# Optimization experiments

Hardware: AMD Instinct MI355X
Metric: run time of the kernel (lower is better)

## Reference

```python
import jax, jax.numpy as jnp
import numpy as np

D = 1024
H = 16
HD = D // H
SCALE = HD ** -0.5
EPS = 1e-5


def _layernorm(x, g, b):
    mu = jnp.mean(x, axis=-1, keepdims=True)
    var = jnp.var(x, axis=-1, keepdims=True)
    return (x - mu) * jax.lax.rsqrt(var + EPS) * g + b


def setup_inputs() -> dict:
    key = jax.random.key(0)
    ks = jax.random.split(key, 10)
    B, L = 2, 2048
    x = jax.random.normal(ks[0], (B, L, D), dtype=jnp.float32)
    s = 1.0 / np.sqrt(D)
    w_qkv = jax.random.normal(ks[1], (D, 3 * D), dtype=jnp.float32) * s
    w_out = jax.random.normal(ks[2], (D, D), dtype=jnp.float32) * s
    w1 = jax.random.normal(ks[3], (D, 2 * D), dtype=jnp.float32) * s
    b1 = jnp.zeros((2 * D,), dtype=jnp.float32)
    w2 = jax.random.normal(ks[4], (2 * D, D), dtype=jnp.float32) / np.sqrt(2 * D)
    b2 = jnp.zeros((D,), dtype=jnp.float32)
    g1 = jnp.ones((D,), dtype=jnp.float32)
    be1 = jnp.zeros((D,), dtype=jnp.float32)
    g2 = jnp.ones((D,), dtype=jnp.float32)
    be2 = jnp.zeros((D,), dtype=jnp.float32)
    return {"x": x, "w_qkv": w_qkv, "w_out": w_out, "w1": w1, "b1": b1,
            "w2": w2, "b2": b2, "g1": g1, "be1": be1, "g2": g2, "be2": be2}


def reference(x, w_qkv, w_out, w1, b1, w2, b2, g1, be1, g2, be2):
    B, L, _ = x.shape
    qkv = (x @ w_qkv).reshape(B, L, 3, H, HD)
    q, k, v = jnp.moveaxis(qkv, 2, 0)          # each [B, L, H, HD]
    # scores: [B, H, L, L]
    attn = jnp.einsum('bqhd,bkhd->bhqk', q, k) * SCALE
    causal = jnp.tril(jnp.ones((L, L), dtype=bool))
    attn = jnp.where(causal[None, None], attn, -jnp.inf)
    attn = jax.nn.softmax(attn, axis=-1)
    out = jnp.einsum('bhqk,bkhd->bqhd', attn, v).reshape(B, L, D)
    out = out @ w_out
    x = _layernorm(x + out, g1, be1)
    ffn = jax.nn.gelu(x @ w1 + b1, approximate=False) @ w2 + b2
    x = _layernorm(x + ffn, g2, be2)
    return x
```

## Files before the change

### kernel.cpp

```cpp
#include <hip/hip_runtime.h>
#include <hip/hip_bf16.h>
#include <math.h>

#define L_SEQ 2048
#define NB 2
#define DM 1024
#define NHEAD 16
#define HDIM 64
#define QKV_LD 3072
#define RL 0.18033688011112042f
#define DTHR 44.3614f

typedef __attribute__((ext_vector_type(8))) __bf16 bf16x8;
typedef __attribute__((ext_vector_type(4))) __bf16 bf16x4;
typedef __attribute__((ext_vector_type(4))) float f32x4;
typedef __attribute__((ext_vector_type(16))) float f32x16;
typedef __attribute__((ext_vector_type(4))) unsigned int u32x4;

typedef __attribute__((address_space(3))) unsigned int lds_u32;
typedef const __attribute__((address_space(1))) unsigned int glob_u32;
#define GLD16(g, l) __builtin_amdgcn_global_load_lds((glob_u32*)(g), (lds_u32*)(l), 16, 0, 0)

__device__ __forceinline__ unsigned pack2(float a, float b) {
  unsigned short ua = __builtin_bit_cast(unsigned short, (__bf16)a);
  unsigned short ub = __builtin_bit_cast(unsigned short, (__bf16)b);
  return (unsigned)ua | ((unsigned)ub << 16);
}

__global__ __launch_bounds__(256) void prep_k(const float* __restrict__ w_qkv,
                                              const float* __restrict__ w_out,
                                              const float* __restrict__ w1,
                                              const float* __restrict__ w2,
                                              const float* __restrict__ x,
                                              __hip_bfloat16* __restrict__ wqT,
                                              __hip_bfloat16* __restrict__ woT,
                                              __hip_bfloat16* __restrict__ w1T,
                                              __hip_bfloat16* __restrict__ w2T,
                                              __hip_bfloat16* __restrict__ xb) {
  const int id = blockIdx.x;
  if (id >= 8192) {
    const size_t base = ((size_t)(id - 8192) * 256 + threadIdx.x) * 8;
    float4 a = *reinterpret_cast<const float4*>(x + base);
    float4 b = *reinterpret_cast<const float4*>(x + base + 4);
    bf16x8 o;
    o[0] = (__bf16)a.x; o[1] = (__bf16)a.y; o[2] = (__bf16)a.z; o[3] = (__bf16)a.w;
    o[4] = (__bf16)b.x; o[5] = (__bf16)b.y; o[6] = (__bf16)b.z; o[7] = (__bf16)b.w;
    *reinterpret_cast<bf16x8*>(xb + base) = o;
    return;
  }
  const float* W; __hip_bfloat16* WT; int K, N, kb, nb;
  if (id < 3072)      { W = w_qkv; WT = wqT; K = 1024; N = 3072; kb = id & 31;          nb = id >> 5; }
  else if (id < 4096) { W = w_out; WT = woT; K = 1024; N = 1024; kb = (id - 3072) & 31; nb = (id - 3072) >> 5; }
  else if (id < 6144) { W = w1;    WT = w1T; K = 1024; N = 2048; kb = (id - 4096) & 31; nb = (id - 4096) >> 5; }
  else                { W = w2;    WT = w2T; K = 2048; N = 1024; kb = (id - 6144) & 63; nb = (id - 6144) >> 6; }
  __shared__ float tsm[32][33];
  const int k0 = kb * 32, n0 = nb * 32;
  const int c = threadIdx.x & 31, r = threadIdx.x >> 5;
#pragma unroll
  for (int i = 0; i < 4; ++i)
    tsm[r + 8 * i][c] = W[(size_t)(k0 + r + 8 * i) * N + n0 + c];
  __syncthreads();
#pragma unroll
  for (int i = 0; i < 4; ++i)
    WT[(size_t)(n0 + r + 8 * i) * K + k0 + c] = __float2bfloat16(tsm[c][r + 8 * i]);
}

template<int EPI, int OUTB, int HASRES, int BN>
__global__ __launch_bounds__(256) void gemm2(const __hip_bfloat16* __restrict__ A,
                                             const __hip_bfloat16* __restrict__ BT,
                                             const float* __restrict__ bias,
                                             float* __restrict__ Cf,
                                             __hip_bfloat16* __restrict__ Cb,
                                             const float* __restrict__ RESF,
                                             const __hip_bfloat16* __restrict__ RESB,
                                             int M, int N, int K) {
  constexpr int MI = (BN == 128) ? 4 : 2;
  __shared__ __align__(16) __hip_bfloat16 As[128 * 64];
  __shared__ __align__(16) __hip_bfloat16 Bs[BN * 64];
  const int tid  = threadIdx.x;
  const int lane = tid & 63, wave = tid >> 6;
  const int wr = (BN == 128) ? (wave >> 1) : wave;
  const int wc = (BN == 128) ? (wave & 1) : 0;
  const int lr = lane & 15, lq = lane >> 4;
  unsigned g = blockIdx.y * gridDim.x + blockIdx.x;
  const unsigned cpx = (gridDim.x * gridDim.y) >> 3;
  g = (g & 7) * cpx + (g >> 3);
  const int bm0 = (int)(g / gridDim.x) * 128;
  const int bn0 = (int)(g % gridDim.x) * BN;
  f32x4 acc[MI][4] = {};

  for (int k0 = 0; k0 < K; k0 += 64) {
#pragma unroll
    for (int j = 0; j < 4; ++j) {
      const int cbase = j * 256 + wave * 64;
      const int c = cbase + lane;
      const int row = c >> 3, slot = c & 7;
      GLD16(A + (size_t)(bm0 + row) * K + k0 + ((slot ^ (row & 7)) * 8),
            (char*)As + cbase * 16);
    }
#pragma unroll
    for (int j = 0; j < BN / 32; ++j) {
      const int cbase = j * 256 + wave * 64;
      const int c = cbase + lane;
      const int row = c >> 3, slot = c & 7;
      GLD16(BT + (size_t)(bn0 + row) * K + k0 + ((slot ^ (row & 7)) * 8),
            (char*)Bs + cbase * 16);
    }
    __syncthreads();
#pragma unroll
    for (int kk = 0; kk < 2; ++kk) {
      const int co = (kk * 64 + lq * 16) ^ ((lr & 7) << 4);
      bf16x8 af[MI], bfr[4];
#pragma unroll
      for (int i = 0; i < MI; ++i)
        af[i] = *reinterpret_cast<const bf16x8*>(
            (const char*)As + (wr * (MI * 16) + i * 16 + lr) * 128 + co);
#pragma unroll
      for (int i = 0; i < 4; ++i)
        bfr[i] = *reinterpret_cast<const bf16x8*>(
            (const char*)Bs + (wc * 64 + i * 16 + lr) * 128 + co);
#pragma unroll
      for (int mi = 0; mi < MI; ++mi)
#pragma unroll
        for (int ni = 0; ni < 4; ++ni)
          acc[mi][ni] = __builtin_amdgcn_mfma_f32_16x16x32_bf16(af[mi], bfr[ni], acc[mi][ni], 0, 0, 0);
    }
    __syncthreads();
  }

#pragma unroll
  for (int mi = 0; mi < MI; ++mi) {
#pragma unroll
    for (int ni = 0; ni < 4; ++ni) {
      const int col = bn0 + wc * 64 + ni * 16 + lr;
      const float bv = (EPI >= 1) ? bias[col] : 0.0f;
#pragma unroll
      for (int j = 0; j < 4; ++j) {
        const int row = bm0 + wr * (MI * 16) + mi * 16 + lq * 4 + j;
        float v = acc[mi][ni][j] + bv;
        if (HASRES == 1) v += RESF[(size_t)row * N + col];
        if (HASRES == 2) v += __bfloat162float(RESB[(size_t)row * N + col]);
        if (EPI == 2) v = 0.5f * v * (1.0f + erff(v * 0.70710678118654752f));
        if (OUTB) Cb[(size_t)row * N + col] = __float2bfloat16(v);
        else      Cf[(size_t)row * N + col] = v;
      }
    }
  }
}


#define DIAG_MASK(sv)                                                               \
  _Pragma("unroll")                                                                 \
  for (int r = 0; r < 16; ++r) {                                                    \
    const int kl = (r & 3) + 8 * (r >> 2) + 4 * hi;                                 \
    if (kl > lq32) sv[r] = -1e30f;                                                  \
  }

#define PV_HALF(wl0, wl1, wh0, wh1, ksg)                                            \
  {                                                                                 \
    unsigned t0_ = hi ? (wl0) : (wh0);                                              \
    unsigned t1_ = hi ? (wl1) : (wh1);                                              \
    t0_ = (unsigned)__shfl_xor((int)t0_, 32);                                       \
    t1_ = (unsigned)__shfl_xor((int)t1_, 32);                                       \
    u32x4 fw;                                                                       \
    fw[0] = hi ? t0_ : (wl0);  fw[1] = hi ? t1_ : (wl1);                            \
    fw[2] = hi ? (wh0) : t0_;  fw[3] = hi ? (wh1) : t1_;                            \
    bf16x8 pfb = __builtin_bit_cast(bf16x8, fw);                                    \
    const int krow_ = (ksg) * 16 + 8 * hi;                                          \
    bf16x8 vA, vB;                                                                  \
    _Pragma("unroll")                                                               \
    for (int j_ = 0; j_ < 8; ++j_) {                                                \
      vA[j_] = VwB[(krow_ + j_) * 64 + lq32];                                       \
      vB[j_] = VwB[(krow_ + j_) * 64 + 32 + lq32];                                  \
    }                                                                               \
    __builtin_amdgcn_s_setprio(1);                                                  \
    o0 = __builtin_amdgcn_mfma_f32_32x32x16_bf16(vA, pfb, o0, 0, 0, 0);             \
    o1 = __builtin_amdgcn_mfma_f32_32x32x16_bf16(vB, pfb, o1, 0, 0, 0);             \
    __builtin_amdgcn_s_setprio(0);                                                  \
  }

__global__ __launch_bounds__(256, 4) void attn_k(const __hip_bfloat16* __restrict__ qkv,
                                                 __hip_bfloat16* __restrict__ outb) {
  __shared__ __align__(16) char smem[4 * 4096 + 2048];
  const int bid = blockIdx.x;
  const int seq = bid >> 3;
  const int bh  = (bid & 7) * 4 + (seq & 3);
  const int qt32 = 63 - (seq >> 2);
  const int b = bh >> 4, h = bh & 15;
  const int qb = qt32 * 32;
  const int tid = threadIdx.x;
  const int lane = tid & 63, wave = tid >> 6;
  const int lq32 = lane & 31, hi = lane >> 5;
  const size_t rowbase = (size_t)(b * L_SEQ) * QKV_LD;
  char* const Vw = smem + wave * 4096;
  const __bf16* const VwB = (const __bf16*)Vw;
  float* const ML = (float*)(smem + 16384);

  bf16x8 qf[4];
  {
    const __hip_bfloat16* qp = qkv + rowbase + (size_t)(qb + lq32) * QKV_LD + h * HDIM + 8 * hi;
#pragma unroll
    for (int c = 0; c < 4; ++c) qf[c] = *reinterpret_cast<const bf16x8*>(qp + 16 * c);
  }

  f32x16 o0 = {}, o1 = {};
  float m = -1e30f, lsum = 0.0f;

  int t = wave;
  bf16x8 kr0, kr1, kr2, kr3;
  if (t <= qt32) {
    const __hip_bfloat16* kp = qkv + rowbase + (size_t)(t * 32 + lq32) * QKV_LD + DM + h * HDIM + 8 * hi;
    kr0 = *reinterpret_cast<const bf16x8*>(kp);
    kr1 = *reinterpret_cast<const bf16x8*>(kp + 16);
    kr2 = *reinterpret_cast<const bf16x8*>(kp + 32);
    kr3 = *reinterpret_cast<const bf16x8*>(kp + 48);
  }

  for (; t <= qt32; t += 4) {
    const int k0 = t * 32;
    const bool pf = (t + 4 <= qt32);
    bf16x8 kn0, kn1, kn2, kn3;
    if (pf) {
      const __hip_bfloat16* kp = qkv + rowbase + (size_t)(k0 + 128 + lq32) * QKV_LD + DM + h * HDIM + 8 * hi;
      kn0 = *reinterpret_cast<const bf16x8*>(kp);
      kn1 = *reinterpret_cast<const bf16x8*>(kp + 16);
      kn2 = *reinterpret_cast<const bf16x8*>(kp + 32);
      kn3 = *reinterpret_cast<const bf16x8*>(kp + 48);
    }
#pragma unroll
    for (int p = 0; p < 4; ++p)
      GLD16(qkv + rowbase + (size_t)(k0 + 8 * p + (lane >> 3)) * QKV_LD + 2 * DM + h * HDIM + (lane & 7) * 8,
            Vw + p * 1024);
    f32x16 s = {};
    __builtin_amdgcn_s_setprio(1);
    s = __builtin_amdgcn_mfma_f32_32x32x16_bf16(kr0, qf[0], s, 0, 0, 0);
    s = __builtin_amdgcn_mfma_f32_32x32x16_bf16(kr1, qf[1], s, 0, 0, 0);
    s = __builtin_amdgcn_mfma_f32_32x32x16_bf16(kr2, qf[2], s, 0, 0, 0);
    s = __builtin_amdgcn_mfma_f32_32x32x16_bf16(kr3, qf[3], s, 0, 0, 0);
    __builtin_amdgcn_s_setprio(0);
    if (t == qt32) { DIAG_MASK(s) }
    float a0 = fmaxf(s[0], s[1]),   a1 = fmaxf(s[2], s[3]);
    float a2 = fmaxf(s[4], s[5]),   a3 = fmaxf(s[6], s[7]);
    float a4 = fmaxf(s[8], s[9]),   a5 = fmaxf(s[10], s[11]);
    float a6 = fmaxf(s[12], s[13]), a7 = fmaxf(s[14], s[15]);
    a0 = fmaxf(a0, a1); a2 = fmaxf(a2, a3); a4 = fmaxf(a4, a5); a6 = fmaxf(a6, a7);
    float tm = fmaxf(fmaxf(a0, a2), fmaxf(a4, a6));
    tm = fmaxf(tm, __shfl_xor(tm, 32));
    if (!__all(tm <= m + DTHR)) {
      const float mn = fmaxf(m, tm);
      const float fac = __builtin_amdgcn_exp2f((m - mn) * RL);
      m = mn; lsum *= fac; o0 *= fac; o1 *= fac;
    }
    const float mneg = -m * RL;
    float rs = 0.0f;
#pragma unroll
    for (int r = 0; r < 16; ++r) {
      s[r] = __builtin_amdgcn_exp2f(fmaf(s[r], RL, mneg));
      rs += s[r];
    }
    rs += __shfl_xor(rs, 32);
    lsum += rs;
    unsigned w0 = pack2(s[0], s[1]),   w1 = pack2(s[2], s[3]);
    unsigned w2 = pack2(s[4], s[5]),   w3 = pack2(s[6], s[7]);
    unsigned w4 = pack2(s[8], s[9]),   w5 = pack2(s[10], s[11]);
    unsigned w6 = pack2(s[12], s[13]), w7 = pack2(s[14], s[15]);
    PV_HALF(w0, w1, w2, w3, 0)
    PV_HALF(w4, w5, w6, w7, 1)
    if (pf) { kr0 = kn0; kr1 = kn1; kr2 = kn2; kr3 = kn3; }
  }

  {
    __bf16* Ow = (__bf16*)Vw;
#pragma unroll
    for (int r = 0; r < 16; ++r) {
      const int d0 = (r & 3) + 8 * (r >> 2) + 4 * hi;
      Ow[d0 * 32 + lq32] = (__bf16)o0[r];
      Ow[(d0 + 32) * 32 + lq32] = (__bf16)o1[r];
    }
    if (hi == 0) {
      ML[wave * 128 + lq32] = m;
      ML[wave * 128 + 64 + lq32] = lsum;
    }
  }
  __syncthreads();

  {
    const int q = tid & 31, dg = tid >> 5;
    const float m0 = ML[q], m1 = ML[128 + q], m2 = ML[256 + q], m3 = ML[384 + q];
    const float M = fmaxf(fmaxf(m0, m1), fmaxf(m2, m3));
    const float c0 = __builtin_amdgcn_exp2f((m0 - M) * RL);
    const float c1 = __builtin_amdgcn_exp2f((m1 - M) * RL);
    const float c2 = __builtin_amdgcn_exp2f((m2 - M) * RL);
    const float c3 = __builtin_amdgcn_exp2f((m3 - M) * RL);
    const float l = c0 * ML[64 + q] + c1 * ML[192 + q] + c2 * ML[320 + q] + c3 * ML[448 + q];
    const float inv = 1.0f / l;
    const __bf16* OB = (const __bf16*)smem;
    bf16x8 ov;
#pragma unroll
    for (int i = 0; i < 8; ++i) {
      const int idx = (dg * 8 + i) * 32 + q;
      const float v = c0 * (float)OB[idx] + c1 * (float)OB[2048 + idx]
                    + c2 * (float)OB[4096 + idx] + c3 * (float)OB[6144 + idx];
      ov[i] = (__bf16)(v * inv);
    }
    *reinterpret_cast<bf16x8*>(outb + (size_t)(b * L_SEQ + qb + q) * DM + h * HDIM + dg * 8) = ov;
  }
}

template<int INB, int OUTB2>
__global__ __launch_bounds__(256) void ln_k(const void* __restrict__ Xv,
                                            const float* __restrict__ g,
                                            const float* __restrict__ be,
                                            float* __restrict__ Y,
                                            __hip_bfloat16* __restrict__ Yb) {
  const int row = blockIdx.x;
  const int tid = threadIdx.x;
  const int lane = tid & 63, wave = tid >> 6;
  float v0, v1, v2, v3;
  if (INB) {
    const __bf16* X = (const __bf16*)Xv;
    bf16x4 x4 = *reinterpret_cast<const bf16x4*>(X + (size_t)row * DM + tid * 4);
    v0 = (float)x4[0]; v1 = (float)x4[1]; v2 = (float)x4[2]; v3 = (float)x4[3];
  } else {
    const float* X = (const float*)Xv;
    float4 x4 = *reinterpret_cast<const float4*>(X + (size_t)row * DM + tid * 4);
    v0 = x4.x; v1 = x4.y; v2 = x4.z; v3 = x4.w;
  }
  float s  = v0 + v1 + v2 + v3;
  float ss = v0 * v0 + v1 * v1 + v2 * v2 + v3 * v3;
#pragma unroll
  for (int off = 1; off < 64; off <<= 1) {
    s  += __shfl_xor(s, off);
    ss += __shfl_xor(ss, off);
  }
  __shared__ float red[8];
  if (lane == 0) { red[wave] = s; red[4 + wave] = ss; }
  __syncthreads();
  float S  = red[0] + red[1] + red[2] + red[3];
  float SS = red[4] + red[5] + red[6] + red[7];
  float mu  = S * (1.0f / DM);
  float var = SS * (1.0f / DM) - mu * mu;
  float rsd = rsqrtf(var + 1e-5f);
  float4 gv = *reinterpret_cast<const float4*>(g + tid * 4);
  float4 bv = *reinterpret_cast<const float4*>(be + tid * 4);
  float4 y;
  y.x = (v0 - mu) * rsd * gv.x + bv.x;
  y.y = (v1 - mu) * rsd * gv.y + bv.y;
  y.z = (v2 - mu) * rsd * gv.z + bv.z;
  y.w = (v3 - mu) * rsd * gv.w + bv.w;
  if (OUTB2) {
    bf16x4 yb;
    yb[0] = (__bf16)y.x; yb[1] = (__bf16)y.y; yb[2] = (__bf16)y.z; yb[3] = (__bf16)y.w;
    *reinterpret_cast<bf16x4*>(Yb + (size_t)row * DM + tid * 4) = yb;
  } else {
    *reinterpret_cast<float4*>(Y + (size_t)row * DM + tid * 4) = y;
  }
}

extern "C" void kernel_launch(void* const* d_in, const int* in_sizes, int n_in,
                              void* d_out, int out_size, void* d_ws, size_t ws_size,
                              hipStream_t stream) {
  const float* x     = (const float*)d_in[0];
  const float* w_qkv = (const float*)d_in[1];
  const float* w_out = (const float*)d_in[2];
  const float* w1    = (const float*)d_in[3];
  const float* b1    = (const float*)d_in[4];
  const float* w2    = (const float*)d_in[5];
  const float* b2    = (const float*)d_in[6];
  const float* g1    = (const float*)d_in[7];
  const float* be1   = (const float*)d_in[8];
  const float* g2    = (const float*)d_in[9];
  const float* be2   = (const float*)d_in[10];
  float* outp = (float*)d_out;
  char* base  = (char*)d_ws;
  const int M = NB * L_SEQ;

  __hip_bfloat16* w2T  = (__hip_bfloat16*)(base + 0);
  __hip_bfloat16* woT  = (__hip_bfloat16*)(base + 4194304);
  __hip_bfloat16* w1T  = (__hip_bfloat16*)(base + 6291456);
  __hip_bfloat16* wqT  = (__hip_bfloat16*)(base + 10485760);
  __hip_bfloat16* xb   = (__hip_bfloat16*)(base + 16777216);
  __hip_bfloat16* qkvb = (__hip_bfloat16*)(base + 25165824);
  __hip_bfloat16* ffh  = (__hip_bfloat16*)(base + 25165824);
  __hip_bfloat16* ln1b = (__hip_bfloat16*)(base + 41943040);
  __hip_bfloat16* projb= (__hip_bfloat16*)(base + 50331648);
  __hip_bfloat16* attnb= (__hip_bfloat16*)(base + 58720256);
  __hip_bfloat16* ffob = (__hip_bfloat16*)(base + 8388608);

  prep_k<<<10240, 256, 0, stream>>>(w_qkv, w_out, w1, w2, x, wqT, woT, w1T, w2T, xb);

  gemm2<0, 1, 0, 128><<<dim3(24, 32), 256, 0, stream>>>(xb, wqT, nullptr, nullptr, qkvb, nullptr, nullptr, M, QKV_LD, DM);
  attn_k<<<2048, 256, 0, stream>>>(qkvb, attnb);
  gemm2<0, 1, 2, 64><<<dim3(16, 32), 256, 0, stream>>>(attnb, woT, nullptr, nullptr, projb, nullptr, xb, M, DM, DM);
  ln_k<1, 1><<<M, 256, 0, stream>>>(projb, g1, be1, nullptr, ln1b);
  gemm2<2, 1, 0, 128><<<dim3(16, 32), 256, 0, stream>>>(ln1b, w1T, b1, nullptr, ffh, nullptr, nullptr, M, 2 * DM, DM);
  gemm2<1, 1, 2, 64><<<dim3(16, 32), 256, 0, stream>>>(ffh, w2T, b2, nullptr, ffob, nullptr, ln1b, M, DM, 2 * DM);
  ln_k<1, 0><<<M, 256, 0, stream>>>(ffob, g2, be2, outp, nullptr);
}
```

Baseline: 191.7 us.

## Process 64-key tiles per wave iteration in causal attention kernel

Measured after the change: 195.3 us. About the same (+1.9%).

```diff
diff --git a/kernel.cpp b/kernel.cpp
--- a/kernel.cpp
+++ b/kernel.cpp
@@ -181,7 +181,7 @@
 
 __global__ __launch_bounds__(256, 4) void attn_k(const __hip_bfloat16* __restrict__ qkv,
                                                  __hip_bfloat16* __restrict__ outb) {
-  __shared__ __align__(16) char smem[4 * 4096 + 2048];
+  __shared__ __align__(16) char smem[4 * 8192 + 2048];
   const int bid = blockIdx.x;
   const int seq = bid >> 3;
   const int bh  = (bid & 7) * 4 + (seq & 3);
@@ -192,9 +192,9 @@
   const int lane = tid & 63, wave = tid >> 6;
   const int lq32 = lane & 31, hi = lane >> 5;
   const size_t rowbase = (size_t)(b * L_SEQ) * QKV_LD;
-  char* const Vw = smem + wave * 4096;
+  char* const Vw = smem + wave * 8192;
   const __bf16* const VwB = (const __bf16*)Vw;
-  float* const ML = (float*)(smem + 16384);
+  float* const ML = (float*)(smem + 32768);
 
   bf16x8 qf[4];
   {
@@ -205,46 +205,53 @@
 
   f32x16 o0 = {}, o1 = {};
   float m = -1e30f, lsum = 0.0f;
-
-  int t = wave;
-  bf16x8 kr0, kr1, kr2, kr3;
-  if (t <= qt32) {
-    const __hip_bfloat16* kp = qkv + rowbase + (size_t)(t * 32 + lq32) * QKV_LD + DM + h * HDIM + 8 * hi;
-    kr0 = *reinterpret_cast<const bf16x8*>(kp);
-    kr1 = *reinterpret_cast<const bf16x8*>(kp + 16);
-    kr2 = *reinterpret_cast<const bf16x8*>(kp + 32);
-    kr3 = *reinterpret_cast<const bf16x8*>(kp + 48);
-  }
-
-  for (; t <= qt32; t += 4) {
-    const int k0 = t * 32;
-    const bool pf = (t + 4 <= qt32);
-    bf16x8 kn0, kn1, kn2, kn3;
-    if (pf) {
-      const __hip_bfloat16* kp = qkv + rowbase + (size_t)(k0 + 128 + lq32) * QKV_LD + DM + h * HDIM + 8 * hi;
-      kn0 = *reinterpret_cast<const bf16x8*>(kp);
-      kn1 = *reinterpret_cast<const bf16x8*>(kp + 16);
-      kn2 = *reinterpret_cast<const bf16x8*>(kp + 32);
-      kn3 = *reinterpret_cast<const bf16x8*>(kp + 48);
-    }
-#pragma unroll
-    for (int p = 0; p < 4; ++p)
+  const int tl = (qb + 31) >> 6;
+
+  for (int t = wave; t <= tl; t += 4) {
+    const int k0 = t * 64;
+    const __hip_bfloat16* kp = qkv + rowbase + (size_t)(k0 + lq32) * QKV_LD + DM + h * HDIM + 8 * hi;
+    bf16x8 kr0 = *reinterpret_cast<const bf16x8*>(kp);
+    bf16x8 kr1 = *reinterpret_cast<const bf16x8*>(kp + 16);
+    bf16x8 kr2 = *reinterpret_cast<const bf16x8*>(kp + 32);
+    bf16x8 kr3 = *reinterpret_cast<const bf16x8*>(kp + 48);
+    const __hip_bfloat16* kp2 = kp + (size_t)32 * QKV_LD;
+    bf16x8 kr4 = *reinterpret_cast<const bf16x8*>(kp2);
+    bf16x8 kr5 = *reinterpret_cast<const bf16x8*>(kp2 + 16);
+    bf16x8 kr6 = *reinterpret_cast<const bf16x8*>(kp2 + 32);
+    bf16x8 kr7 = *reinterpret_cast<const bf16x8*>(kp2 + 48);
+#pragma unroll
+    for (int p = 0; p < 8; ++p)
       GLD16(qkv + rowbase + (size_t)(k0 + 8 * p + (lane >> 3)) * QKV_LD + 2 * DM + h * HDIM + (lane & 7) * 8,
             Vw + p * 1024);
-    f32x16 s = {};
+    f32x16 s0 = {}, s1 = {};
     __builtin_amdgcn_s_setprio(1);
-    s = __builtin_amdgcn_mfma_f32_32x32x16_bf16(kr0, qf[0], s, 0, 0, 0);
-    s = __builtin_amdgcn_mfma_f32_32x32x16_bf16(kr1, qf[1], s, 0, 0, 0);
-    s = __builtin_amdgcn_mfma_f32_32x32x16_bf16(kr2, qf[2], s, 0, 0, 0);
-    s = __builtin_amdgcn_mfma_f32_32x32x16_bf16(kr3, qf[3], s, 0, 0, 0);
+    s0 = __builtin_amdgcn_mfma_f32_32x32x16_bf16(kr0, qf[0], s0, 0, 0, 0);
+    s0 = __builtin_amdgcn_mfma_f32_32x32x16_bf16(kr1, qf[1], s0, 0, 0, 0);
+    s0 = __builtin_amdgcn_mfma_f32_32x32x16_bf16(kr2, qf[2], s0, 0, 0, 0);
+    s0 = __builtin_amdgcn_mfma_f32_32x32x16_bf16(kr3, qf[3], s0, 0, 0, 0);
+    s1 = __builtin_amdgcn_mfma_f32_32x32x16_bf16(kr4, qf[0], s1, 0, 0, 0);
+    s1 = __builtin_amdgcn_mfma_f32_32x32x16_bf16(kr5, qf[1], s1, 0, 0, 0);
+    s1 = __builtin_amdgcn_mfma_f32_32x32x16_bf16(kr6, qf[2], s1, 0, 0, 0);
+    s1 = __builtin_amdgcn_mfma_f32_32x32x16_bf16(kr7, qf[3], s1, 0, 0, 0);
     __builtin_amdgcn_s_setprio(0);
-    if (t == qt32) { DIAG_MASK(s) }
-    float a0 = fmaxf(s[0], s[1]),   a1 = fmaxf(s[2], s[3]);
-    float a2 = fmaxf(s[4], s[5]),   a3 = fmaxf(s[6], s[7]);
-    float a4 = fmaxf(s[8], s[9]),   a5 = fmaxf(s[10], s[11]);
-    float a6 = fmaxf(s[12], s[13]), a7 = fmaxf(s[14], s[15]);
-    a0 = fmaxf(a0, a1); a2 = fmaxf(a2, a3); a4 = fmaxf(a4, a5); a6 = fmaxf(a6, a7);
-    float tm = fmaxf(fmaxf(a0, a2), fmaxf(a4, a6));
+    if (t == tl) {
+      if (qt32 & 1) { DIAG_MASK(s1) }
+      else {
+        DIAG_MASK(s0)
+#pragma unroll
+        for (int r = 0; r < 16; ++r) s1[r] = -1e30f;
+      }
+    }
+    float a0 = fmaxf(fmaxf(s0[0], s0[1]),   fmaxf(s0[2], s0[3]));
+    float a1 = fmaxf(fmaxf(s0[4], s0[5]),   fmaxf(s0[6], s0[7]));
+    float a2 = fmaxf(fmaxf(s0[8], s0[9]),   fmaxf(s0[10], s0[11]));
+    float a3 = fmaxf(fmaxf(s0[12], s0[13]), fmaxf(s0[14], s0[15]));
+    float a4 = fmaxf(fmaxf(s1[0], s1[1]),   fmaxf(s1[2], s1[3]));
+    float a5 = fmaxf(fmaxf(s1[4], s1[5]),   fmaxf(s1[6], s1[7]));
+    float a6 = fmaxf(fmaxf(s1[8], s1[9]),   fmaxf(s1[10], s1[11]));
+    float a7 = fmaxf(fmaxf(s1[12], s1[13]), fmaxf(s1[14], s1[15]));
+    float tm = fmaxf(fmaxf(fmaxf(a0, a1), fmaxf(a2, a3)),
+                     fmaxf(fmaxf(a4, a5), fmaxf(a6, a7)));
     tm = fmaxf(tm, __shfl_xor(tm, 32));
     if (!__all(tm <= m + DTHR)) {
       const float mn = fmaxf(m, tm);
@@ -255,18 +262,32 @@
     float rs = 0.0f;
 #pragma unroll
     for (int r = 0; r < 16; ++r) {
-      s[r] = __builtin_amdgcn_exp2f(fmaf(s[r], RL, mneg));
-      rs += s[r];
+      s0[r] = __builtin_amdgcn_exp2f(fmaf(s0[r], RL, mneg));
+      rs += s0[r];
+    }
+    {
+      unsigned w0 = pack2(s0[0], s0[1]),   w1 = pack2(s0[2], s0[3]);
+      unsigned w2 = pack2(s0[4], s0[5]),   w3 = pack2(s0[6], s0[7]);
+      unsigned w4 = pack2(s0[8], s0[9]),   w5 = pack2(s0[10], s0[11]);
+      unsigned w6 = pack2(s0[12], s0[13]), w7 = pack2(s0[14], s0[15]);
+      PV_HALF(w0, w1, w2, w3, 0)
+      PV_HALF(w4, w5, w6, w7, 1)
+    }
+#pragma unroll
+    for (int r = 0; r < 16; ++r) {
+      s1[r] = __builtin_amdgcn_exp2f(fmaf(s1[r], RL, mneg));
+      rs += s1[r];
+    }
+    {
+      unsigned w0 = pack2(s1[0], s1[1]),   w1 = pack2(s1[2], s1[3]);
+      unsigned w2 = pack2(s1[4], s1[5]),   w3 = pack2(s1[6], s1[7]);
+      unsigned w4 = pack2(s1[8], s1[9]),   w5 = pack2(s1[10], s1[11]);
+      unsigned w6 = pack2(s1[12], s1[13]), w7 = pack2(s1[14], s1[15]);
+      PV_HALF(w0, w1, w2, w3, 2)
+      PV_HALF(w4, w5, w6, w7, 3)
     }
     rs += __shfl_xor(rs, 32);
     lsum += rs;
-    unsigned w0 = pack2(s[0], s[1]),   w1 = pack2(s[2], s[3]);
-    unsigned w2 = pack2(s[4], s[5]),   w3 = pack2(s[6], s[7]);
-    unsigned w4 = pack2(s[8], s[9]),   w5 = pack2(s[10], s[11]);
-    unsigned w6 = pack2(s[12], s[13]), w7 = pack2(s[14], s[15]);
-    PV_HALF(w0, w1, w2, w3, 0)
-    PV_HALF(w4, w5, w6, w7, 1)
-    if (pf) { kr0 = kn0; kr1 = kn1; kr2 = kn2; kr3 = kn3; }
   }
 
   {
@@ -299,8 +320,8 @@
 #pragma unroll
     for (int i = 0; i < 8; ++i) {
       const int idx = (dg * 8 + i) * 32 + q;
-      const float v = c0 * (float)OB[idx] + c1 * (float)OB[2048 + idx]
-                    + c2 * (float)OB[4096 + idx] + c3 * (float)OB[6144 + idx];
+      const float v = c0 * (float)OB[idx] + c1 * (float)OB[4096 + idx]
+                    + c2 * (float)OB[8192 + idx] + c3 * (float)OB[12288 + idx];
       ov[i] = (__bf16)(v * inv);
     }
     *reinterpret_cast<bf16x8*>(outb + (size_t)(b * L_SEQ + qb + q) * DM + h * HDIM + dg * 8) = ov;
```
